# Kernel optimization log

Measured on AMD Instinct MI355X. Metric: run time of the kernel, lower is better.

The kernel has to match this reference:

```python
import jax, jax.numpy as jnp
import numpy as np

N_NODES = 100000
N_EDGES = 3200000
D_FEAT = 512
HIDDEN = 16
N_CLASSES = 40


def gcn_conv(x, edge_index, edge_weight, W, b):
    """PyG GCNConv: add self-loops, symmetric norm, gather-weight-scatter, linear."""
    n = x.shape[0]
    row, col = edge_index[0], edge_index[1]
    loop = jnp.arange(n, dtype=edge_index.dtype)
    row = jnp.concatenate([row, loop])
    col = jnp.concatenate([col, loop])
    w = jnp.concatenate([edge_weight, jnp.ones((n,), dtype=edge_weight.dtype)])
    # gcn_norm: deg over target nodes (col), norm = d^-1/2[row] * w * d^-1/2[col]
    deg = jax.ops.segment_sum(w, col, num_segments=n)
    dinv = jnp.where(deg > 0, jax.lax.rsqrt(deg), 0.0)
    norm = dinv[row] * w * dinv[col]
    h = x @ W                                   # [N, out] small GEMM
    msg = norm[:, None] * h[row]                # gather + scale  [E+N, out]
    out = jax.ops.segment_sum(msg, col, num_segments=n)  # scatter-add
    return out + b


def setup_inputs() -> dict:
    key = jax.random.key(0)
    ks = jax.random.split(key, 6)
    x = jax.random.normal(ks[0], (N_NODES, D_FEAT), dtype=jnp.float32)
    edge_index = jax.random.randint(ks[1], (2, N_EDGES), 0, N_NODES, dtype=jnp.int32)
    edge_weight = jax.random.uniform(ks[2], (N_EDGES,), dtype=jnp.float32)
    W1 = jax.random.normal(ks[3], (D_FEAT, HIDDEN), dtype=jnp.float32) * (1.0 / np.sqrt(D_FEAT))
    b1 = jnp.zeros((HIDDEN,), dtype=jnp.float32)
    W2 = jax.random.normal(ks[4], (HIDDEN, N_CLASSES), dtype=jnp.float32) * (1.0 / np.sqrt(HIDDEN))
    b2 = jnp.zeros((N_CLASSES,), dtype=jnp.float32)
    return {"x": x, "edge_index": edge_index, "edge_weight": edge_weight,
            "W1": W1, "b1": b1, "W2": W2, "b2": b2}


def reference(x, edge_index, edge_weight, W1, b1, W2, b2):
    h = jax.nn.relu(gcn_conv(x, edge_index, edge_weight, W1, b1))
    # dropout omitted (eval mode / deterministic baseline)
    return gcn_conv(h, edge_index, edge_weight, W2, b2)
```

## Files before the change

kernel.cpp:

```cpp
#include <hip/hip_runtime.h>
#include <hip/hip_bf16.h>

#define N_NODES 100000
#define N_EDGES 3200000
#define D_FEAT  512
#define HIDDEN  16
#define NCLS    40

__global__ __launch_bounds__(256) void k_init_deg(float* __restrict__ deg) {
    int i = blockIdx.x * blockDim.x + threadIdx.x;
    if (i < N_NODES) deg[i] = 1.0f;
}

__global__ __launch_bounds__(256) void k_deg(const int* __restrict__ col,
                                             const float* __restrict__ w,
                                             float* __restrict__ deg) {
    int e = blockIdx.x * blockDim.x + threadIdx.x;
    if (e < N_EDGES) atomicAdd(&deg[col[e]], w[e]);
}

__global__ __launch_bounds__(256) void k_dinv(float* __restrict__ deg) {
    int i = blockIdx.x * blockDim.x + threadIdx.x;
    if (i < N_NODES) deg[i] = 1.0f / sqrtf(deg[i]);
}

__global__ __launch_bounds__(256) void k_gemm1(const float* __restrict__ x,
                                               const float* __restrict__ W,
                                               float* __restrict__ h) {
    const int lane = threadIdx.x & 63;
    const int wave = (blockIdx.x * blockDim.x + threadIdx.x) >> 6;
    const int nw   = (gridDim.x * blockDim.x) >> 6;

    float wA[4][16], wB[4][16];
#pragma unroll
    for (int j = 0; j < 4; ++j)
#pragma unroll
        for (int c = 0; c < 16; ++c) {
            wA[j][c] = W[(4 * lane + j) * 16 + c];
            wB[j][c] = W[(256 + 4 * lane + j) * 16 + c];
        }

    for (int r = wave; r < N_NODES; r += nw) {
        const float4* xr = (const float4*)(x + (long long)r * D_FEAT);
        float4 xa = xr[lane];
        float4 xb = xr[lane + 64];
        float acc[16];
#pragma unroll
        for (int c = 0; c < 16; ++c)
            acc[c] = xa.x * wA[0][c] + xa.y * wA[1][c] + xa.z * wA[2][c] + xa.w * wA[3][c]
                   + xb.x * wB[0][c] + xb.y * wB[1][c] + xb.z * wB[2][c] + xb.w * wB[3][c];

        float a8[8];
        {
            const bool up = lane & 1;
#pragma unroll
            for (int i = 0; i < 8; ++i) {
                float send = up ? acc[i] : acc[i + 8];
                float keep = up ? acc[i + 8] : acc[i];
                a8[i] = keep + __shfl_xor(send, 1, 64);
            }
        }
        float a4[4];
        {
            const bool up = lane & 2;
#pragma unroll
            for (int i = 0; i < 4; ++i) {
                float send = up ? a8[i] : a8[i + 4];
                float keep = up ? a8[i + 4] : a8[i];
                a4[i] = keep + __shfl_xor(send, 2, 64);
            }
        }
        float a2[2];
        {
            const bool up = lane & 4;
#pragma unroll
            for (int i = 0; i < 2; ++i) {
                float send = up ? a2[i] * 0.0f + a4[i] : a4[i + 2];
                (void)send;
            }
            float s0 = up ? a4[0] : a4[2];
            float k0 = up ? a4[2] : a4[0];
            float s1 = up ? a4[1] : a4[3];
            float k1 = up ? a4[3] : a4[1];
            a2[0] = k0 + __shfl_xor(s0, 4, 64);
            a2[1] = k1 + __shfl_xor(s1, 4, 64);
        }
        float v;
        {
            const bool up = lane & 8;
            float send = up ? a2[0] : a2[1];
            float keep = up ? a2[1] : a2[0];
            v = keep + __shfl_xor(send, 8, 64);
        }
        v += __shfl_xor(v, 16, 64);
        v += __shfl_xor(v, 32, 64);

        if (lane < 16) {
            int c = ((lane & 1) << 3) | ((lane & 2) << 1) | ((lane & 4) >> 1) | ((lane & 8) >> 3);
            h[(long long)r * HIDDEN + c] = v;
        }
    }
}

__global__ __launch_bounds__(256) void k_self1(const float* __restrict__ h1,
                                               const float* __restrict__ dinv,
                                               const float* __restrict__ b,
                                               float* __restrict__ out1) {
    int idx = blockIdx.x * blockDim.x + threadIdx.x;
    if (idx < N_NODES * HIDDEN) {
        int i = idx >> 4, c = idx & 15;
        float d = dinv[i];
        out1[idx] = d * d * h1[idx] + b[c];
    }
}

__global__ __launch_bounds__(256) void k_scat1(const int* __restrict__ row,
                                               const int* __restrict__ col,
                                               const float* __restrict__ w,
                                               const float* __restrict__ dinv,
                                               const float* __restrict__ h1,
                                               float* __restrict__ out1) {
    const int total = N_EDGES * HIDDEN;
    const int stride = gridDim.x * blockDim.x;
    for (int idx = blockIdx.x * blockDim.x + threadIdx.x; idx < total; idx += stride) {
        int e = idx >> 4, c = idx & 15;
        int r = row[e], t = col[e];
        float nrm = dinv[r] * w[e] * dinv[t];
        atomicAdd(&out1[t * HIDDEN + c], nrm * h1[r * HIDDEN + c]);
    }
}

__global__ __launch_bounds__(256) void k_gemm2(const float* __restrict__ out1,
                                               const float* __restrict__ W2,
                                               float* __restrict__ h2) {
    __shared__ float Ws[HIDDEN * NCLS];
    for (int i = threadIdx.x; i < HIDDEN * NCLS; i += blockDim.x) Ws[i] = W2[i];
    __syncthreads();
    const int total = N_NODES * NCLS;
    const int stride = gridDim.x * blockDim.x;
    for (int idx = blockIdx.x * blockDim.x + threadIdx.x; idx < total; idx += stride) {
        int i = idx / NCLS, c = idx - i * NCLS;
        const float* r = out1 + i * HIDDEN;
        float s = 0.0f;
#pragma unroll
        for (int k = 0; k < HIDDEN; ++k) {
            float v = r[k];
            v = v > 0.0f ? v : 0.0f;
            s += v * Ws[k * NCLS + c];
        }
        h2[idx] = s;
    }
}

__global__ __launch_bounds__(256) void k_self2(const float* __restrict__ h2,
                                               const float* __restrict__ dinv,
                                               const float* __restrict__ b,
                                               float* __restrict__ out) {
    const int total = N_NODES * NCLS;
    const int stride = gridDim.x * blockDim.x;
    for (int idx = blockIdx.x * blockDim.x + threadIdx.x; idx < total; idx += stride) {
        int i = idx / NCLS, c = idx - i * NCLS;
        float d = dinv[i];
        out[idx] = d * d * h2[idx] + b[c];
    }
}

__global__ __launch_bounds__(256) void k_scat2(const int* __restrict__ row,
                                               const int* __restrict__ col,
                                               const float* __restrict__ w,
                                               const float* __restrict__ dinv,
                                               const float* __restrict__ h2,
                                               float* __restrict__ out) {
    const int total = N_EDGES * NCLS;
    const int stride = gridDim.x * blockDim.x;
    for (int idx = blockIdx.x * blockDim.x + threadIdx.x; idx < total; idx += stride) {
        int e = idx / NCLS, c = idx - e * NCLS;
        int r = row[e], t = col[e];
        float nrm = dinv[r] * w[e] * dinv[t];
        atomicAdd(&out[t * NCLS + c], nrm * h2[r * NCLS + c]);
    }
}

extern "C" void kernel_launch(void* const* d_in, const int* in_sizes, int n_in,
                              void* d_out, int out_size, void* d_ws, size_t ws_size,
                              hipStream_t stream) {
    const float* x   = (const float*)d_in[0];
    const int*   ei  = (const int*)d_in[1];
    const float* ew  = (const float*)d_in[2];
    const float* W1  = (const float*)d_in[3];
    const float* b1  = (const float*)d_in[4];
    const float* W2  = (const float*)d_in[5];
    const float* b2  = (const float*)d_in[6];
    const int* row = ei;
    const int* col = ei + N_EDGES;
    float* out = (float*)d_out;

    char* ws = (char*)d_ws;
    float* dinv = (float*)(ws);
    float* h1   = (float*)(ws + (1u << 20));
    float* out1 = (float*)(ws + 9u * (1u << 20));
    float* h2   = (float*)(ws + 17u * (1u << 20));

    k_init_deg<<<(N_NODES + 255) / 256, 256, 0, stream>>>(dinv);
    k_deg<<<(N_EDGES + 255) / 256, 256, 0, stream>>>(col, ew, dinv);
    k_dinv<<<(N_NODES + 255) / 256, 256, 0, stream>>>(dinv);

    k_gemm1<<<1024, 256, 0, stream>>>(x, W1, h1);

    k_self1<<<(N_NODES * HIDDEN + 255) / 256, 256, 0, stream>>>(h1, dinv, b1, out1);
    k_scat1<<<4096, 256, 0, stream>>>(row, col, ew, dinv, h1, out1);

    k_gemm2<<<4096, 256, 0, stream>>>(out1, W2, h2);

    k_self2<<<4096, 256, 0, stream>>>(h2, dinv, b2, out);
    k_scat2<<<8192, 256, 0, stream>>>(row, col, ew, dinv, h2, out);
}
```

Baseline: 1.201 ms.

## Build CSR by target and replace atomic scatters with per-node gathers

Builds a CSR grouped by target node (count, scan, fill) with the normalized edge weights precomputed. Both layers then run as atomic-free gathers over 16-wide features. The second layer aggregates before the 16x40 linear map (A·(hW) = (A·h)·W), so the costly 40-wide atomic scatter becomes a 16-wide gather followed by a small GEMM with bias. This adds CSR build work and random writes during fill. The floating-point summation order also changes.

```diff
diff --git a/kernel.cpp b/kernel.cpp
--- a/kernel.cpp
+++ b/kernel.cpp
@@ -6,6 +6,7 @@
 #define D_FEAT  512
 #define HIDDEN  16
 #define NCLS    40
+#define SCAN_BLOCKS ((N_NODES + 255) / 256)
 
 __global__ __launch_bounds__(256) void k_init_deg(float* __restrict__ deg) {
     int i = blockIdx.x * blockDim.x + threadIdx.x;
@@ -22,6 +23,76 @@
 __global__ __launch_bounds__(256) void k_dinv(float* __restrict__ deg) {
     int i = blockIdx.x * blockDim.x + threadIdx.x;
     if (i < N_NODES) deg[i] = 1.0f / sqrtf(deg[i]);
+}
+
+__global__ __launch_bounds__(256) void k_zero_cnt(int* __restrict__ cnt) {
+    int i = blockIdx.x * blockDim.x + threadIdx.x;
+    if (i < N_NODES) cnt[i] = 0;
+}
+
+__global__ __launch_bounds__(256) void k_count(const int* __restrict__ col,
+                                               int* __restrict__ cnt) {
+    int e = blockIdx.x * blockDim.x + threadIdx.x;
+    if (e < N_EDGES) atomicAdd(&cnt[col[e]], 1);
+}
+
+__global__ __launch_bounds__(256) void k_scan1(const int* __restrict__ cnt,
+                                               int* __restrict__ off,
+                                               int* __restrict__ bsum) {
+    __shared__ int s[256];
+    int t = threadIdx.x;
+    int i = blockIdx.x * 256 + t;
+    int v = (i < N_NODES) ? cnt[i] : 0;
+    s[t] = v;
+    __syncthreads();
+#pragma unroll
+    for (int d = 1; d < 256; d <<= 1) {
+        int x = (t >= d) ? s[t - d] : 0;
+        __syncthreads();
+        s[t] += x;
+        __syncthreads();
+    }
+    if (i < N_NODES) off[i] = s[t] - v;
+    if (t == 255) bsum[blockIdx.x] = s[255];
+}
+
+__global__ void k_scan2(int* __restrict__ bsum, int* __restrict__ off) {
+    if (threadIdx.x == 0 && blockIdx.x == 0) {
+        int run = 0;
+        for (int b = 0; b < SCAN_BLOCKS; ++b) {
+            int v = bsum[b];
+            bsum[b] = run;
+            run += v;
+        }
+        off[N_NODES] = N_EDGES;
+    }
+}
+
+__global__ __launch_bounds__(256) void k_scan3(int* __restrict__ off,
+                                               const int* __restrict__ bsum,
+                                               int* __restrict__ cursor) {
+    int i = blockIdx.x * 256 + threadIdx.x;
+    if (i < N_NODES) {
+        int v = off[i] + bsum[blockIdx.x];
+        off[i] = v;
+        cursor[i] = v;
+    }
+}
+
+__global__ __launch_bounds__(256) void k_fill(const int* __restrict__ row,
+                                              const int* __restrict__ col,
+                                              const float* __restrict__ w,
+                                              const float* __restrict__ dinv,
+                                              int* __restrict__ cursor,
+                                              int* __restrict__ src,
+                                              float* __restrict__ val) {
+    int e = blockIdx.x * blockDim.x + threadIdx.x;
+    if (e < N_EDGES) {
+        int r = row[e], t = col[e];
+        int p = atomicAdd(&cursor[t], 1);
+        src[p] = r;
+        val[p] = dinv[r] * w[e] * dinv[t];
+    }
 }
 
 __global__ __launch_bounds__(256) void k_gemm1(const float* __restrict__ x,
@@ -73,11 +144,6 @@
         float a2[2];
         {
             const bool up = lane & 4;
-#pragma unroll
-            for (int i = 0; i < 2; ++i) {
-                float send = up ? a2[i] * 0.0f + a4[i] : a4[i + 2];
-                (void)send;
-            }
             float s0 = up ? a4[0] : a4[2];
             float k0 = up ? a4[2] : a4[0];
             float s1 = up ? a4[1] : a4[3];
@@ -102,82 +168,54 @@
     }
 }
 
-__global__ __launch_bounds__(256) void k_self1(const float* __restrict__ h1,
-                                               const float* __restrict__ dinv,
-                                               const float* __restrict__ b,
-                                               float* __restrict__ out1) {
-    int idx = blockIdx.x * blockDim.x + threadIdx.x;
-    if (idx < N_NODES * HIDDEN) {
-        int i = idx >> 4, c = idx & 15;
-        float d = dinv[i];
-        out1[idx] = d * d * h1[idx] + b[c];
-    }
-}
-
-__global__ __launch_bounds__(256) void k_scat1(const int* __restrict__ row,
-                                               const int* __restrict__ col,
-                                               const float* __restrict__ w,
-                                               const float* __restrict__ dinv,
-                                               const float* __restrict__ h1,
-                                               float* __restrict__ out1) {
-    const int total = N_EDGES * HIDDEN;
-    const int stride = gridDim.x * blockDim.x;
-    for (int idx = blockIdx.x * blockDim.x + threadIdx.x; idx < total; idx += stride) {
-        int e = idx >> 4, c = idx & 15;
-        int r = row[e], t = col[e];
-        float nrm = dinv[r] * w[e] * dinv[t];
-        atomicAdd(&out1[t * HIDDEN + c], nrm * h1[r * HIDDEN + c]);
-    }
-}
-
-__global__ __launch_bounds__(256) void k_gemm2(const float* __restrict__ out1,
+__global__ __launch_bounds__(256) void k_gather(const int* __restrict__ off,
+                                                const int* __restrict__ src,
+                                                const float* __restrict__ val,
+                                                const float* __restrict__ h,
+                                                const float* __restrict__ dinv,
+                                                const float* __restrict__ bias,
+                                                float* __restrict__ out,
+                                                int relu_out) {
+    const int lane = threadIdx.x & 63;
+    const int c = lane & 15, j = lane >> 4;
+    const int wave = (blockIdx.x * blockDim.x + threadIdx.x) >> 6;
+    const int nw   = (gridDim.x * blockDim.x) >> 6;
+
+    for (int t = wave; t < N_NODES; t += nw) {
+        const int s0 = off[t], s1 = off[t + 1];
+        float acc = 0.0f;
+        for (int p = s0 + j; p < s1; p += 4) {
+            int r = src[p];
+            float nv = val[p];
+            acc += nv * h[r * HIDDEN + c];
+        }
+        acc += __shfl_xor(acc, 16, 64);
+        acc += __shfl_xor(acc, 32, 64);
+        if (lane < 16) {
+            float d = dinv[t];
+            float v = acc + d * d * h[t * HIDDEN + c];
+            if (bias) v += bias[c];
+            if (relu_out) v = v > 0.0f ? v : 0.0f;
+            out[t * HIDDEN + c] = v;
+        }
+    }
+}
+
+__global__ __launch_bounds__(256) void k_gemm2(const float* __restrict__ agg,
                                                const float* __restrict__ W2,
-                                               float* __restrict__ h2) {
+                                               const float* __restrict__ b2,
+                                               float* __restrict__ out) {
     __shared__ float Ws[HIDDEN * NCLS];
     for (int i = threadIdx.x; i < HIDDEN * NCLS; i += blockDim.x) Ws[i] = W2[i];
     __syncthreads();
-    const int total = N_NODES * NCLS;
-    const int stride = gridDim.x * blockDim.x;
-    for (int idx = blockIdx.x * blockDim.x + threadIdx.x; idx < total; idx += stride) {
+    int idx = blockIdx.x * blockDim.x + threadIdx.x;
+    if (idx < N_NODES * NCLS) {
         int i = idx / NCLS, c = idx - i * NCLS;
-        const float* r = out1 + i * HIDDEN;
-        float s = 0.0f;
-#pragma unroll
-        for (int k = 0; k < HIDDEN; ++k) {
-            float v = r[k];
-            v = v > 0.0f ? v : 0.0f;
-            s += v * Ws[k * NCLS + c];
-        }
-        h2[idx] = s;
-    }
-}
-
-__global__ __launch_bounds__(256) void k_self2(const float* __restrict__ h2,
-                                               const float* __restrict__ dinv,
-                                               const float* __restrict__ b,
-                                               float* __restrict__ out) {
-    const int total = N_NODES * NCLS;
-    const int stride = gridDim.x * blockDim.x;
-    for (int idx = blockIdx.x * blockDim.x + threadIdx.x; idx < total; idx += stride) {
-        int i = idx / NCLS, c = idx - i * NCLS;
-        float d = dinv[i];
-        out[idx] = d * d * h2[idx] + b[c];
-    }
-}
-
-__global__ __launch_bounds__(256) void k_scat2(const int* __restrict__ row,
-                                               const int* __restrict__ col,
-                                               const float* __restrict__ w,
-                                               const float* __restrict__ dinv,
-                                               const float* __restrict__ h2,
-                                               float* __restrict__ out) {
-    const int total = N_EDGES * NCLS;
-    const int stride = gridDim.x * blockDim.x;
-    for (int idx = blockIdx.x * blockDim.x + threadIdx.x; idx < total; idx += stride) {
-        int e = idx / NCLS, c = idx - e * NCLS;
-        int r = row[e], t = col[e];
-        float nrm = dinv[r] * w[e] * dinv[t];
-        atomicAdd(&out[t * NCLS + c], nrm * h2[r * NCLS + c]);
+        const float* r = agg + i * HIDDEN;
+        float s = b2[c];
+#pragma unroll
+        for (int k = 0; k < HIDDEN; ++k) s += r[k] * Ws[k * NCLS + c];
+        out[idx] = s;
     }
 }
 
@@ -196,22 +234,35 @@
     float* out = (float*)d_out;
 
     char* ws = (char*)d_ws;
-    float* dinv = (float*)(ws);
-    float* h1   = (float*)(ws + (1u << 20));
-    float* out1 = (float*)(ws + 9u * (1u << 20));
-    float* h2   = (float*)(ws + 17u * (1u << 20));
-
-    k_init_deg<<<(N_NODES + 255) / 256, 256, 0, stream>>>(dinv);
-    k_deg<<<(N_EDGES + 255) / 256, 256, 0, stream>>>(col, ew, dinv);
-    k_dinv<<<(N_NODES + 255) / 256, 256, 0, stream>>>(dinv);
+    float* dinv   = (float*)(ws);
+    int*   cnt    = (int*)  (ws +  1u * (1u << 19));
+    int*   off    = (int*)  (ws +  2u * (1u << 19));
+    int*   bsum   = (int*)  (ws +  3u * (1u << 19));
+    int*   src    = (int*)  (ws +  2u * (1u << 20));
+    float* val    = (float*)(ws + 15u * (1u << 20));
+    float* h1     = (float*)(ws + 28u * (1u << 20));
+    float* hrelu  = (float*)(ws + 35u * (1u << 20));
+    int*   cursor = cnt;
+    float* agg2   = h1;
+
+    const int EB = (N_EDGES + 255) / 256;
+
+    k_init_deg<<<SCAN_BLOCKS, 256, 0, stream>>>(dinv);
+    k_deg<<<EB, 256, 0, stream>>>(col, ew, dinv);
+    k_dinv<<<SCAN_BLOCKS, 256, 0, stream>>>(dinv);
+
+    k_zero_cnt<<<SCAN_BLOCKS, 256, 0, stream>>>(cnt);
+    k_count<<<EB, 256, 0, stream>>>(col, cnt);
+    k_scan1<<<SCAN_BLOCKS, 256, 0, stream>>>(cnt, off, bsum);
+    k_scan2<<<1, 64, 0, stream>>>(bsum, off);
+    k_scan3<<<SCAN_BLOCKS, 256, 0, stream>>>(off, bsum, cursor);
+    k_fill<<<EB, 256, 0, stream>>>(row, col, ew, dinv, cursor, src, val);
 
     k_gemm1<<<1024, 256, 0, stream>>>(x, W1, h1);
 
-    k_self1<<<(N_NODES * HIDDEN + 255) / 256, 256, 0, stream>>>(h1, dinv, b1, out1);
-    k_scat1<<<4096, 256, 0, stream>>>(row, col, ew, dinv, h1, out1);
-
-    k_gemm2<<<4096, 256, 0, stream>>>(out1, W2, h2);
-
-    k_self2<<<4096, 256, 0, stream>>>(h2, dinv, b2, out);
-    k_scat2<<<8192, 256, 0, stream>>>(row, col, ew, dinv, h2, out);
-}
+    k_gather<<<2048, 256, 0, stream>>>(off, src, val, h1, dinv, b1, hrelu, 1);
+
+    k_gather<<<2048, 256, 0, stream>>>(off, src, val, hrelu, dinv, nullptr, agg2, 0);
+
+    k_gemm2<<<(N_NODES * NCLS + 255) / 256, 256, 0, stream>>>(agg2, W2, b2, out);
+}
```

After: 1.019 ms. 1.18x faster.
